# Performance work log

Hardware: AMD Instinct MI355X
Metric: run time of the kernel (lower is better)

Reference implementation:

```python
import jax, jax.numpy as jnp
import numpy as np

N = 20000        # nodes
E = 160000       # directed edges (self-loops added in reference, as PyG GATConv does)
IN = 128         # in_channels
OUT = 128        # out_channels
H = 36           # heads of conv1 (head kwarg)
C = 36           # per-head channels of conv1 (== head kwarg)
HID = H * C      # 1296, conv1 concat output
NEG_SLOPE = 0.2  # PyG GATConv default


def gat_layer(x, src, dst, W, a_src, a_dst, bias, heads, ch, concat, num_nodes):
    """One PyG-style GATConv (eval mode, self-loops already in src/dst)."""
    h = (x @ W).reshape(num_nodes, heads, ch)               # [N,H,C]
    alpha_s = jnp.sum(h * a_src, axis=-1)                   # [N,H]
    alpha_d = jnp.sum(h * a_dst, axis=-1)                   # [N,H]
    e = jax.nn.leaky_relu(alpha_s[src] + alpha_d[dst], NEG_SLOPE)  # [E,H]
    # segment softmax over incoming edges of each target node
    m = jax.ops.segment_max(e, dst, num_segments=num_nodes)        # [N,H]
    m = jnp.where(jnp.isfinite(m), m, 0.0)                  # nodes with no in-edges
    ex = jnp.exp(e - m[dst])                                # [E,H]
    denom = jax.ops.segment_sum(ex, dst, num_segments=num_nodes)   # [N,H]
    alpha = ex / (denom[dst] + 1e-16)                       # [E,H]
    # weighted scatter-aggregate of source features
    out = jax.ops.segment_sum(h[src] * alpha[:, :, None], dst, num_segments=num_nodes)  # [N,H,C]
    out = out.reshape(num_nodes, heads * ch) if concat else out.mean(axis=1)
    return out + bias


def setup_inputs() -> dict:
    key = jax.random.key(0)
    ks = jax.random.split(key, 12)
    x = jax.random.normal(ks[0], (N, IN), jnp.float32)
    edge_index = jax.random.randint(ks[1], (2, E), 0, N, dtype=jnp.int64)
    # conv1 params: heads=36, out per head=36, concat
    W1 = jax.random.normal(ks[2], (IN, H * C), jnp.float32) / np.float32(np.sqrt(IN))
    a_src1 = jax.random.normal(ks[3], (H, C), jnp.float32) * 0.1
    a_dst1 = jax.random.normal(ks[4], (H, C), jnp.float32) * 0.1
    b1 = jnp.zeros((HID,), jnp.float32)
    # conv2 params: heads=1, out=OUT, no concat
    W2 = jax.random.normal(ks[5], (HID, OUT), jnp.float32) / np.float32(np.sqrt(HID))
    a_src2 = jax.random.normal(ks[6], (1, OUT), jnp.float32) * 0.1
    a_dst2 = jax.random.normal(ks[7], (1, OUT), jnp.float32) * 0.1
    b2 = jnp.zeros((OUT,), jnp.float32)
    return {"x": x, "edge_index": edge_index,
            "W1": W1, "a_src1": a_src1, "a_dst1": a_dst1, "b1": b1,
            "W2": W2, "a_src2": a_src2, "a_dst2": a_dst2, "b2": b2}


def reference(x, edge_index, W1, a_src1, a_dst1, b1, W2, a_src2, a_dst2, b2):
    num_nodes = x.shape[0]
    loop = jnp.arange(num_nodes, dtype=edge_index.dtype)
    src = jnp.concatenate([edge_index[0], loop])   # add self-loops (PyG default)
    dst = jnp.concatenate([edge_index[1], loop])
    h = jax.nn.relu(gat_layer(x, src, dst, W1, a_src1, a_dst1, b1,
                              heads=H, ch=C, concat=True, num_nodes=num_nodes))
    out = jax.nn.relu(gat_layer(h, src, dst, W2, a_src2, a_dst2, b2,
                                heads=1, ch=OUT, concat=False, num_nodes=num_nodes))
    return out
```

## Files before the change

kernel.cpp:

```cpp
#include <hip/hip_runtime.h>

#define N_NODES 20000
#define E_EDGES 160000
#define ET (E_EDGES + N_NODES)
#define IN_CH 128
#define HID 1296
#define HEADS 36
#define CPH 36
#define OUT_CH 128
#define KP2 1344
#define NEG_SLOPE 0.2f

typedef __attribute__((ext_vector_type(8))) short bf16x8;
typedef __attribute__((ext_vector_type(8))) unsigned short ushort8;
typedef __attribute__((ext_vector_type(4))) float floatx4;

__device__ __forceinline__ float bf2f(unsigned short u) {
    union { unsigned int i; float f; } c; c.i = ((unsigned int)u) << 16; return c.f;
}
__device__ __forceinline__ unsigned short f2bf(float f) {
    union { float f; unsigned int i; } c; c.f = f;
    unsigned int r = c.i + 0x7FFF + ((c.i >> 16) & 1);
    return (unsigned short)(r >> 16);
}

#define NX (N_NODES * IN_CH / 4)
#define NW1 (HID * IN_CH)
#define NW2 (OUT_CH * KP2)
#define NPREP (NX + NW1 + NW2)
__global__ __launch_bounds__(256) void k_prepcnt(const float* __restrict__ x,
                                                 unsigned short* __restrict__ xb,
                                                 const float* __restrict__ W1,
                                                 unsigned short* __restrict__ W1T,
                                                 const float* __restrict__ W2,
                                                 unsigned short* __restrict__ W2T,
                                                 const int* __restrict__ ei,
                                                 int* __restrict__ cnt) {
    int gid = blockIdx.x * 256 + threadIdx.x;
    if (gid < NX) {
        float4 v = ((const float4*)x)[gid];
        ushort4 o; o.x = f2bf(v.x); o.y = f2bf(v.y); o.z = f2bf(v.z); o.w = f2bf(v.w);
        ((ushort4*)xb)[gid] = o;
    } else if (gid < NX + NW1) {
        int g = gid - NX;
        int n = g >> 7, k = g & 127;
        W1T[g] = f2bf(W1[(size_t)k * HID + n]);
    } else if (gid < NPREP) {
        int g = gid - NX - NW1;
        int n = g / KP2, k = g - n * KP2;
        W2T[g] = (k < HID) ? f2bf(W2[(size_t)k * OUT_CH + n]) : 0;
    } else if (gid < NPREP + ET) {
        int e = gid - NPREP;
        int d = (e < E_EDGES) ? ei[E_EDGES + e] : (e - E_EDGES);
        atomicAdd(&cnt[d], 1);
    }
}

__global__ __launch_bounds__(256) void k_gemm1(const unsigned short* __restrict__ xb,
                                               const unsigned short* __restrict__ W1T,
                                               unsigned short* __restrict__ h1b) {
    __shared__ unsigned short As[128][136];
    __shared__ unsigned short Bs[64][136];
    int tid = threadIdx.x;
    int r0 = blockIdx.x * 128;
    int n0 = blockIdx.y * 64;
#pragma unroll
    for (int i = 0; i < 8; i++) {
        int c = tid + i * 256;
        int row = c >> 4, kc = (c & 15) * 8;
        int gr = min(r0 + row, N_NODES - 1);
        *(bf16x8*)&As[row][kc] = *(const bf16x8*)(xb + (size_t)gr * IN_CH + kc);
    }
#pragma unroll
    for (int i = 0; i < 4; i++) {
        int c = tid + i * 256;
        int row = c >> 4, kc = (c & 15) * 8;
        int gn = min(n0 + row, HID - 1);
        *(bf16x8*)&Bs[row][kc] = *(const bf16x8*)(W1T + (size_t)gn * IN_CH + kc);
    }
    __syncthreads();
    int lane = tid & 63, w = tid >> 6;
    int quad = lane >> 4, l15 = lane & 15;
    int mbase = w * 32;
    floatx4 acc[2][4];
#pragma unroll
    for (int i = 0; i < 2; i++)
#pragma unroll
        for (int j = 0; j < 4; j++) acc[i][j] = (floatx4){0.f, 0.f, 0.f, 0.f};
#pragma unroll
    for (int kc = 0; kc < 128; kc += 32) {
        bf16x8 a0 = *(const bf16x8*)&As[mbase + l15][kc + quad * 8];
        bf16x8 a1 = *(const bf16x8*)&As[mbase + 16 + l15][kc + quad * 8];
#pragma unroll
        for (int j = 0; j < 4; j++) {
            bf16x8 b = *(const bf16x8*)&Bs[j * 16 + l15][kc + quad * 8];
            acc[0][j] = __builtin_amdgcn_mfma_f32_16x16x32_bf16(a0, b, acc[0][j], 0, 0, 0);
            acc[1][j] = __builtin_amdgcn_mfma_f32_16x16x32_bf16(a1, b, acc[1][j], 0, 0, 0);
        }
    }
#pragma unroll
    for (int i = 0; i < 2; i++)
#pragma unroll
        for (int j = 0; j < 4; j++) {
            int colc = n0 + j * 16 + l15;
            if (colc >= HID) continue;
#pragma unroll
            for (int r = 0; r < 4; r++) {
                int row = r0 + mbase + i * 16 + quad * 4 + r;
                if (row < N_NODES)
                    h1b[(size_t)row * HID + colc] = f2bf(acc[i][j][r]);
            }
        }
}

__global__ __launch_bounds__(256) void k_gemm2(const unsigned short* __restrict__ A,
                                               const unsigned short* __restrict__ W2T,
                                               float* __restrict__ h2a,
                                               float* __restrict__ h2b) {
    __shared__ unsigned short As[32][40];
    __shared__ unsigned short Bs[128][40];
    int tid = threadIdx.x;
    int r0 = blockIdx.x * 32;
    int kbase = blockIdx.y * 672;
    int lane = tid & 63, w = tid >> 6;
    int quad = lane >> 4, l15 = lane & 15;
    int nbase = w * 32;
    floatx4 acc[2][2];
#pragma unroll
    for (int i = 0; i < 2; i++)
#pragma unroll
        for (int j = 0; j < 2; j++) acc[i][j] = (floatx4){0.f, 0.f, 0.f, 0.f};

    for (int it = 0; it < 21; it++) {
        int k0 = kbase + it * 32;
        __syncthreads();
        if (tid < 128) {
            int row = tid >> 2, kc = (tid & 3) * 8;
            *(bf16x8*)&As[row][kc] = *(const bf16x8*)(A + (size_t)(r0 + row) * KP2 + k0 + kc);
        }
#pragma unroll
        for (int i = 0; i < 2; i++) {
            int c = tid + i * 256;
            int row = c >> 2, kc = (c & 3) * 8;
            *(bf16x8*)&Bs[row][kc] = *(const bf16x8*)(W2T + (size_t)row * KP2 + k0 + kc);
        }
        __syncthreads();
        bf16x8 a0 = *(const bf16x8*)&As[l15][quad * 8];
        bf16x8 a1 = *(const bf16x8*)&As[16 + l15][quad * 8];
        bf16x8 b0 = *(const bf16x8*)&Bs[nbase + l15][quad * 8];
        bf16x8 b1 = *(const bf16x8*)&Bs[nbase + 16 + l15][quad * 8];
        acc[0][0] = __builtin_amdgcn_mfma_f32_16x16x32_bf16(a0, b0, acc[0][0], 0, 0, 0);
        acc[1][0] = __builtin_amdgcn_mfma_f32_16x16x32_bf16(a1, b0, acc[1][0], 0, 0, 0);
        acc[0][1] = __builtin_amdgcn_mfma_f32_16x16x32_bf16(a0, b1, acc[0][1], 0, 0, 0);
        acc[1][1] = __builtin_amdgcn_mfma_f32_16x16x32_bf16(a1, b1, acc[1][1], 0, 0, 0);
    }
    float* dst = (blockIdx.y == 0) ? h2a : h2b;
#pragma unroll
    for (int i = 0; i < 2; i++)
#pragma unroll
        for (int j = 0; j < 2; j++) {
            int colc = nbase + j * 16 + l15;
#pragma unroll
            for (int r = 0; r < 4; r++) {
                int row = r0 + i * 16 + quad * 4 + r;
                dst[(size_t)row * OUT_CH + colc] = acc[i][j][r];
            }
        }
}

__global__ __launch_bounds__(256) void k_alpha1(const unsigned short* __restrict__ h1b,
                                                const float* __restrict__ a_src,
                                                const float* __restrict__ a_dst,
                                                float* __restrict__ as,
                                                float* __restrict__ ad) {
    __shared__ float s_a[HEADS * CPH], s_b[HEADS * CPH];
    int tid = threadIdx.x;
    for (int i = tid; i < HEADS * CPH; i += 256) { s_a[i] = a_src[i]; s_b[i] = a_dst[i]; }
    __syncthreads();
    int gid = blockIdx.x * 256 + tid;
    if (gid >= N_NODES * HEADS) return;
    int n = gid / HEADS, h = gid - n * HEADS;
    const unsigned short* row = h1b + (size_t)n * HID + h * CPH;
    float ss = 0.f, sd = 0.f;
#pragma unroll
    for (int c = 0; c < CPH; c += 2) {
        uint u = *(const uint*)(row + c);
        float v0 = bf2f((unsigned short)(u & 0xFFFF));
        float v1 = bf2f((unsigned short)(u >> 16));
        ss += v0 * s_a[h * CPH + c] + v1 * s_a[h * CPH + c + 1];
        sd += v0 * s_b[h * CPH + c] + v1 * s_b[h * CPH + c + 1];
    }
    as[gid] = ss;
    ad[gid] = sd;
}

__global__ __launch_bounds__(1024) void k_scan(const int* __restrict__ cnt, int* __restrict__ rowp) {
    __shared__ int sh[1024];
    const int PER = 20;
    int t = threadIdx.x;
    int base = t * PER;
    int local[PER];
    int sum = 0;
    for (int i = 0; i < PER; i++) {
        int idx = base + i;
        int v = (idx < N_NODES) ? cnt[idx] : 0;
        local[i] = sum;
        sum += v;
    }
    sh[t] = sum;
    __syncthreads();
    for (int off = 1; off < 1024; off <<= 1) {
        int v = (t >= off) ? sh[t - off] : 0;
        __syncthreads();
        sh[t] += v;
        __syncthreads();
    }
    int offset = (t == 0) ? 0 : sh[t - 1];
    for (int i = 0; i < PER; i++) {
        int idx = base + i;
        if (idx < N_NODES) rowp[idx] = offset + local[i];
    }
    if (t == 1023) rowp[N_NODES] = sh[1023];
}

__global__ void k_fill(const int* __restrict__ ei, const int* __restrict__ rowp,
                       int* __restrict__ cursor, int* __restrict__ col,
                       int* __restrict__ dstn) {
    int e = blockIdx.x * 256 + threadIdx.x;
    if (e >= ET) return;
    int s, d;
    if (e < E_EDGES) { s = ei[e]; d = ei[E_EDGES + e]; }
    else { s = e - E_EDGES; d = s; }
    int pos = rowp[d] + atomicAdd(&cursor[d], 1);
    col[pos] = s;
    dstn[pos] = d;
}

__global__ __launch_bounds__(256) void k_w1(const float* __restrict__ as1,
                                            const float* __restrict__ ad1,
                                            const int* __restrict__ col,
                                            const int* __restrict__ dstn,
                                            float* __restrict__ w,
                                            float* __restrict__ den) {
    int gid = blockIdx.x * 256 + threadIdx.x;
    if (gid >= ET * HEADS) return;
    int p = gid / HEADS, h = gid - p * HEADS;
    int s = col[p], d = dstn[p];
    float v = as1[(size_t)s * HEADS + h] + ad1[(size_t)d * HEADS + h];
    v = (v > 0.f) ? v : NEG_SLOPE * v;
    float ev = __expf(v);
    w[gid] = ev;
    atomicAdd(&den[(size_t)d * HEADS + h], ev);
}

__global__ __launch_bounds__(192) void k_agg1(const unsigned short* __restrict__ h1b,
                                              const float* __restrict__ w,
                                              const float* __restrict__ den,
                                              const int* __restrict__ rowp,
                                              const int* __restrict__ col,
                                              const float* __restrict__ b1,
                                              unsigned short* __restrict__ out1b) {
    int n = blockIdx.x;
    int tid = threadIdx.x;
    int r0 = rowp[n], r1 = rowp[n + 1];
    const bool act = tid < 162;
    int c0 = tid * 8;
    int h0 = act ? c0 / 36 : 0;
    int h7 = act ? (c0 + 7) / 36 : 0;
    int split = (h0 + 1) * 36 - c0;
    float sel[8];
#pragma unroll
    for (int j = 0; j < 8; j++) sel[j] = (j < split) ? 0.f : 1.f;
    float inv0 = 0.f, inv7 = 0.f;
    if (act) {
        inv0 = 1.f / (den[(size_t)n * HEADS + h0] + 1e-16f);
        inv7 = (h7 == h0) ? inv0 : 1.f / (den[(size_t)n * HEADS + h7] + 1e-16f);
    }
    float acc[8];
#pragma unroll
    for (int j = 0; j < 8; j++) acc[j] = 0.f;

    if (act) {
        int e = r0;
        for (; e + 4 <= r1; e += 4) {
            int s0 = col[e], s1 = col[e + 1], s2 = col[e + 2], s3 = col[e + 3];
            float wA0 = w[(size_t)(e + 0) * HEADS + h0] * inv0;
            float wB0 = w[(size_t)(e + 0) * HEADS + h7] * inv7;
            float wA1 = w[(size_t)(e + 1) * HEADS + h0] * inv0;
            float wB1 = w[(size_t)(e + 1) * HEADS + h7] * inv7;
            float wA2 = w[(size_t)(e + 2) * HEADS + h0] * inv0;
            float wB2 = w[(size_t)(e + 2) * HEADS + h7] * inv7;
            float wA3 = w[(size_t)(e + 3) * HEADS + h0] * inv0;
            float wB3 = w[(size_t)(e + 3) * HEADS + h7] * inv7;
            ushort8 v0 = *(const ushort8*)(h1b + (size_t)s0 * HID + c0);
            ushort8 v1 = *(const ushort8*)(h1b + (size_t)s1 * HID + c0);
            ushort8 v2 = *(const ushort8*)(h1b + (size_t)s2 * HID + c0);
            ushort8 v3 = *(const ushort8*)(h1b + (size_t)s3 * HID + c0);
            float dw0 = wB0 - wA0, dw1 = wB1 - wA1, dw2 = wB2 - wA2, dw3 = wB3 - wA3;
#pragma unroll
            for (int j = 0; j < 8; j++) {
                acc[j] = fmaf(fmaf(sel[j], dw0, wA0), bf2f(v0[j]), acc[j]);
                acc[j] = fmaf(fmaf(sel[j], dw1, wA1), bf2f(v1[j]), acc[j]);
                acc[j] = fmaf(fmaf(sel[j], dw2, wA2), bf2f(v2[j]), acc[j]);
                acc[j] = fmaf(fmaf(sel[j], dw3, wA3), bf2f(v3[j]), acc[j]);
            }
        }
        for (; e < r1; e++) {
            int s = col[e];
            float wA = w[(size_t)e * HEADS + h0] * inv0;
            float wB = w[(size_t)e * HEADS + h7] * inv7;
            ushort8 vv = *(const ushort8*)(h1b + (size_t)s * HID + c0);
            float dw = wB - wA;
#pragma unroll
            for (int j = 0; j < 8; j++)
                acc[j] = fmaf(fmaf(sel[j], dw, wA), bf2f(vv[j]), acc[j]);
        }
    }
    if (tid < KP2 / 8) {
        ushort8 o;
        if (act) {
#pragma unroll
            for (int j = 0; j < 8; j++) {
                float vv = acc[j] + b1[c0 + j];
                o[j] = f2bf(fmaxf(vv, 0.f));
            }
        } else {
#pragma unroll
            for (int j = 0; j < 8; j++) o[j] = 0;
        }
        *(ushort8*)(out1b + (size_t)n * KP2 + c0) = o;
    }
}

__global__ __launch_bounds__(64) void k_alpha2c(const float* __restrict__ h2a,
                                                const float* __restrict__ h2b,
                                                unsigned short* __restrict__ h2q,
                                                const float* __restrict__ a_src,
                                                const float* __restrict__ a_dst,
                                                float* __restrict__ as,
                                                float* __restrict__ ad) {
    int n = blockIdx.x;
    int t = threadIdx.x;
    size_t base = (size_t)n * OUT_CH;
    float v0 = h2a[base + t] + h2b[base + t];
    float v1 = h2a[base + t + 64] + h2b[base + t + 64];
    h2q[base + t] = f2bf(v0);
    h2q[base + t + 64] = f2bf(v1);
    float ss = v0 * a_src[t] + v1 * a_src[t + 64];
    float sd = v0 * a_dst[t] + v1 * a_dst[t + 64];
    for (int off = 32; off > 0; off >>= 1) {
        ss += __shfl_down(ss, off);
        sd += __shfl_down(sd, off);
    }
    if (t == 0) { as[n] = ss; ad[n] = sd; }
}

__global__ __launch_bounds__(64) void k_agg2(const unsigned short* __restrict__ h2q,
                                             const float* __restrict__ as,
                                             const float* __restrict__ ad,
                                             const int* __restrict__ rowp,
                                             const int* __restrict__ col,
                                             const float* __restrict__ b2,
                                             float* __restrict__ out) {
    int n = blockIdx.x;
    int t = threadIdx.x;
    int r0 = rowp[n], r1 = rowp[n + 1];
    float adn = ad[n];
    float den = 0.f;
    for (int e = r0 + t; e < r1; e += 64) {
        float v = as[col[e]] + adn;
        v = (v > 0.f) ? v : NEG_SLOPE * v;
        den += __expf(v);
    }
#pragma unroll
    for (int off = 32; off > 0; off >>= 1) den += __shfl_xor(den, off);
    float inv = 1.f / (den + 1e-16f);
    __shared__ float wsh[32];
    __shared__ int csh[32];
    float acc0 = 0.f, acc1 = 0.f;
    for (int p0 = r0; p0 < r1; p0 += 32) {
        int ne = min(32, r1 - p0);
        __syncthreads();
        if (t < ne) {
            int s = col[p0 + t];
            csh[t] = s;
            float v = as[s] + adn;
            v = (v > 0.f) ? v : NEG_SLOPE * v;
            wsh[t] = __expf(v) * inv;
        }
        __syncthreads();
        int e = 0;
        for (; e + 4 <= ne; e += 4) {
            uint u0 = *(const uint*)(h2q + (size_t)csh[e + 0] * OUT_CH + t * 2);
            uint u1 = *(const uint*)(h2q + (size_t)csh[e + 1] * OUT_CH + t * 2);
            uint u2 = *(const uint*)(h2q + (size_t)csh[e + 2] * OUT_CH + t * 2);
            uint u3 = *(const uint*)(h2q + (size_t)csh[e + 3] * OUT_CH + t * 2);
            float w0 = wsh[e], w1 = wsh[e + 1], w2 = wsh[e + 2], w3 = wsh[e + 3];
            acc0 += w0 * bf2f((unsigned short)(u0 & 0xFFFF)) + w1 * bf2f((unsigned short)(u1 & 0xFFFF))
                  + w2 * bf2f((unsigned short)(u2 & 0xFFFF)) + w3 * bf2f((unsigned short)(u3 & 0xFFFF));
            acc1 += w0 * bf2f((unsigned short)(u0 >> 16)) + w1 * bf2f((unsigned short)(u1 >> 16))
                  + w2 * bf2f((unsigned short)(u2 >> 16)) + w3 * bf2f((unsigned short)(u3 >> 16));
        }
        for (; e < ne; e++) {
            uint ua = *(const uint*)(h2q + (size_t)csh[e] * OUT_CH + t * 2);
            float wa = wsh[e];
            acc0 += wa * bf2f((unsigned short)(ua & 0xFFFF));
            acc1 += wa * bf2f((unsigned short)(ua >> 16));
        }
    }
    float o0 = acc0 + b2[t * 2];
    float o1 = acc1 + b2[t * 2 + 1];
    out[(size_t)n * OUT_CH + t * 2]     = (o0 > 0.f) ? o0 : 0.f;
    out[(size_t)n * OUT_CH + t * 2 + 1] = (o1 > 0.f) ? o1 : 0.f;
}

extern "C" void kernel_launch(void* const* d_in, const int* in_sizes, int n_in,
                              void* d_out, int out_size, void* d_ws, size_t ws_size,
                              hipStream_t stream) {
    const float* x      = (const float*)d_in[0];
    const int*   ei     = (const int*)d_in[1];
    const float* W1     = (const float*)d_in[2];
    const float* a_src1 = (const float*)d_in[3];
    const float* a_dst1 = (const float*)d_in[4];
    const float* b1     = (const float*)d_in[5];
    const float* W2     = (const float*)d_in[6];
    const float* a_src2 = (const float*)d_in[7];
    const float* a_dst2 = (const float*)d_in[8];
    const float* b2     = (const float*)d_in[9];
    float* out = (float*)d_out;

    unsigned short* h1b   = (unsigned short*)d_ws;
    unsigned short* out1b = h1b + (size_t)N_NODES * HID;
    unsigned short* xb    = out1b + (size_t)N_NODES * KP2;
    unsigned short* W1T   = xb + (size_t)N_NODES * IN_CH;
    unsigned short* W2T   = W1T + (size_t)HID * IN_CH;
    float* fbase = (float*)(W2T + NW2);
    float* as1  = fbase;
    float* ad1  = as1 + (size_t)N_NODES * HEADS;
    float* wbuf = ad1 + (size_t)N_NODES * HEADS;
    float* h2a  = wbuf;
    float* h2b  = wbuf + (size_t)N_NODES * OUT_CH;
    unsigned short* h2q = (unsigned short*)(wbuf + (size_t)2 * N_NODES * OUT_CH);
    float* as2  = wbuf + (size_t)ET * HEADS;
    float* ad2  = as2 + N_NODES;
    int* cnt    = (int*)(ad2 + N_NODES);
    int* cursor = cnt + N_NODES;
    float* den1 = (float*)(cursor + N_NODES);
    int* rowp   = (int*)(den1 + (size_t)N_NODES * HEADS);
    int* colx   = rowp + (N_NODES + 1);
    int* dstn   = colx + ET;

    hipMemsetAsync(cnt, 0, (size_t)(2 * N_NODES + N_NODES * HEADS) * sizeof(int), stream);

    k_prepcnt<<<(NPREP + ET + 255) / 256, 256, 0, stream>>>(x, xb, W1, W1T, W2, W2T, ei, cnt);
    k_scan<<<1, 1024, 0, stream>>>(cnt, rowp);
    k_fill<<<(ET + 255) / 256, 256, 0, stream>>>(ei, rowp, cursor, colx, dstn);
    k_gemm1<<<dim3(157, 21), 256, 0, stream>>>(xb, W1T, h1b);
    k_alpha1<<<(N_NODES * HEADS + 255) / 256, 256, 0, stream>>>(h1b, a_src1, a_dst1, as1, ad1);
    k_w1<<<(ET * HEADS + 255) / 256, 256, 0, stream>>>(as1, ad1, colx, dstn, wbuf, den1);
    k_agg1<<<N_NODES, 192, 0, stream>>>(h1b, wbuf, den1, rowp, colx, b1, out1b);
    k_gemm2<<<dim3(625, 2), 256, 0, stream>>>(out1b, W2T, h2a, h2b);
    k_alpha2c<<<N_NODES, 64, 0, stream>>>(h2a, h2b, h2q, a_src2, a_dst2, as2, ad2);
    k_agg2<<<N_NODES, 64, 0, stream>>>(h2q, as2, ad2, rowp, colx, b2, out);
}
```

Baseline: 316.5 us.

## Fuse attention-weight softmax into aggregation kernels with deferred normalization

Removes the separate per-edge-per-head weight kernel and its atomic denominator accumulation. Layer-1 aggregation now computes exp(leaky_relu(as+ad)) inline from node-level scores and normalizes by the accumulated sum at the end. Layer-2 aggregation likewise drops its separate denominator pass and normalizes after accumulation. This saves a large weight buffer write/read, atomics and a memset, at the cost of recomputing exponentials redundantly across threads in each block.

```diff
diff --git a/kernel.cpp b/kernel.cpp
--- a/kernel.cpp
+++ b/kernel.cpp
@@ -22,6 +22,9 @@
     union { float f; unsigned int i; } c; c.f = f;
     unsigned int r = c.i + 0x7FFF + ((c.i >> 16) & 1);
     return (unsigned short)(r >> 16);
+}
+__device__ __forceinline__ float lrelu(float v) {
+    return (v > 0.f) ? v : NEG_SLOPE * v;
 }
 
 #define NX (N_NODES * IN_CH / 4)
@@ -224,8 +227,7 @@
 }
 
 __global__ void k_fill(const int* __restrict__ ei, const int* __restrict__ rowp,
-                       int* __restrict__ cursor, int* __restrict__ col,
-                       int* __restrict__ dstn) {
+                       int* __restrict__ cursor, int* __restrict__ col) {
     int e = blockIdx.x * 256 + threadIdx.x;
     if (e >= ET) return;
     int s, d;
@@ -233,29 +235,11 @@
     else { s = e - E_EDGES; d = s; }
     int pos = rowp[d] + atomicAdd(&cursor[d], 1);
     col[pos] = s;
-    dstn[pos] = d;
-}
-
-__global__ __launch_bounds__(256) void k_w1(const float* __restrict__ as1,
-                                            const float* __restrict__ ad1,
-                                            const int* __restrict__ col,
-                                            const int* __restrict__ dstn,
-                                            float* __restrict__ w,
-                                            float* __restrict__ den) {
-    int gid = blockIdx.x * 256 + threadIdx.x;
-    if (gid >= ET * HEADS) return;
-    int p = gid / HEADS, h = gid - p * HEADS;
-    int s = col[p], d = dstn[p];
-    float v = as1[(size_t)s * HEADS + h] + ad1[(size_t)d * HEADS + h];
-    v = (v > 0.f) ? v : NEG_SLOPE * v;
-    float ev = __expf(v);
-    w[gid] = ev;
-    atomicAdd(&den[(size_t)d * HEADS + h], ev);
 }
 
 __global__ __launch_bounds__(192) void k_agg1(const unsigned short* __restrict__ h1b,
-                                              const float* __restrict__ w,
-                                              const float* __restrict__ den,
+                                              const float* __restrict__ as1,
+                                              const float* __restrict__ ad1,
                                               const int* __restrict__ rowp,
                                               const int* __restrict__ col,
                                               const float* __restrict__ b1,
@@ -271,31 +255,34 @@
     float sel[8];
 #pragma unroll
     for (int j = 0; j < 8; j++) sel[j] = (j < split) ? 0.f : 1.f;
-    float inv0 = 0.f, inv7 = 0.f;
+    float ad0 = 0.f, ad7 = 0.f;
     if (act) {
-        inv0 = 1.f / (den[(size_t)n * HEADS + h0] + 1e-16f);
-        inv7 = (h7 == h0) ? inv0 : 1.f / (den[(size_t)n * HEADS + h7] + 1e-16f);
+        ad0 = ad1[(size_t)n * HEADS + h0];
+        ad7 = (h7 == h0) ? ad0 : ad1[(size_t)n * HEADS + h7];
     }
     float acc[8];
 #pragma unroll
     for (int j = 0; j < 8; j++) acc[j] = 0.f;
+    float sA = 0.f, sB = 0.f;
 
     if (act) {
         int e = r0;
         for (; e + 4 <= r1; e += 4) {
             int s0 = col[e], s1 = col[e + 1], s2 = col[e + 2], s3 = col[e + 3];
-            float wA0 = w[(size_t)(e + 0) * HEADS + h0] * inv0;
-            float wB0 = w[(size_t)(e + 0) * HEADS + h7] * inv7;
-            float wA1 = w[(size_t)(e + 1) * HEADS + h0] * inv0;
-            float wB1 = w[(size_t)(e + 1) * HEADS + h7] * inv7;
-            float wA2 = w[(size_t)(e + 2) * HEADS + h0] * inv0;
-            float wB2 = w[(size_t)(e + 2) * HEADS + h7] * inv7;
-            float wA3 = w[(size_t)(e + 3) * HEADS + h0] * inv0;
-            float wB3 = w[(size_t)(e + 3) * HEADS + h7] * inv7;
+            float wA0 = __expf(lrelu(as1[(size_t)s0 * HEADS + h0] + ad0));
+            float wB0 = __expf(lrelu(as1[(size_t)s0 * HEADS + h7] + ad7));
+            float wA1 = __expf(lrelu(as1[(size_t)s1 * HEADS + h0] + ad0));
+            float wB1 = __expf(lrelu(as1[(size_t)s1 * HEADS + h7] + ad7));
+            float wA2 = __expf(lrelu(as1[(size_t)s2 * HEADS + h0] + ad0));
+            float wB2 = __expf(lrelu(as1[(size_t)s2 * HEADS + h7] + ad7));
+            float wA3 = __expf(lrelu(as1[(size_t)s3 * HEADS + h0] + ad0));
+            float wB3 = __expf(lrelu(as1[(size_t)s3 * HEADS + h7] + ad7));
             ushort8 v0 = *(const ushort8*)(h1b + (size_t)s0 * HID + c0);
             ushort8 v1 = *(const ushort8*)(h1b + (size_t)s1 * HID + c0);
             ushort8 v2 = *(const ushort8*)(h1b + (size_t)s2 * HID + c0);
             ushort8 v3 = *(const ushort8*)(h1b + (size_t)s3 * HID + c0);
+            sA += wA0 + wA1 + wA2 + wA3;
+            sB += wB0 + wB1 + wB2 + wB3;
             float dw0 = wB0 - wA0, dw1 = wB1 - wA1, dw2 = wB2 - wA2, dw3 = wB3 - wA3;
 #pragma unroll
             for (int j = 0; j < 8; j++) {
@@ -307,9 +294,10 @@
         }
         for (; e < r1; e++) {
             int s = col[e];
-            float wA = w[(size_t)e * HEADS + h0] * inv0;
-            float wB = w[(size_t)e * HEADS + h7] * inv7;
+            float wA = __expf(lrelu(as1[(size_t)s * HEADS + h0] + ad0));
+            float wB = __expf(lrelu(as1[(size_t)s * HEADS + h7] + ad7));
             ushort8 vv = *(const ushort8*)(h1b + (size_t)s * HID + c0);
+            sA += wA; sB += wB;
             float dw = wB - wA;
 #pragma unroll
             for (int j = 0; j < 8; j++)
@@ -319,9 +307,12 @@
     if (tid < KP2 / 8) {
         ushort8 o;
         if (act) {
+            float invA = 1.f / (sA + 1e-16f);
+            float invB = 1.f / (sB + 1e-16f);
+            float dinv = invB - invA;
 #pragma unroll
             for (int j = 0; j < 8; j++) {
-                float vv = acc[j] + b1[c0 + j];
+                float vv = acc[j] * fmaf(sel[j], dinv, invA) + b1[c0 + j];
                 o[j] = f2bf(fmaxf(vv, 0.f));
             }
         } else {
@@ -366,27 +357,17 @@
     int t = threadIdx.x;
     int r0 = rowp[n], r1 = rowp[n + 1];
     float adn = ad[n];
-    float den = 0.f;
-    for (int e = r0 + t; e < r1; e += 64) {
-        float v = as[col[e]] + adn;
-        v = (v > 0.f) ? v : NEG_SLOPE * v;
-        den += __expf(v);
-    }
-#pragma unroll
-    for (int off = 32; off > 0; off >>= 1) den += __shfl_xor(den, off);
-    float inv = 1.f / (den + 1e-16f);
     __shared__ float wsh[32];
     __shared__ int csh[32];
     float acc0 = 0.f, acc1 = 0.f;
+    float sw = 0.f;
     for (int p0 = r0; p0 < r1; p0 += 32) {
         int ne = min(32, r1 - p0);
         __syncthreads();
         if (t < ne) {
             int s = col[p0 + t];
             csh[t] = s;
-            float v = as[s] + adn;
-            v = (v > 0.f) ? v : NEG_SLOPE * v;
-            wsh[t] = __expf(v) * inv;
+            wsh[t] = __expf(lrelu(as[s] + adn));
         }
         __syncthreads();
         int e = 0;
@@ -396,6 +377,7 @@
             uint u2 = *(const uint*)(h2q + (size_t)csh[e + 2] * OUT_CH + t * 2);
             uint u3 = *(const uint*)(h2q + (size_t)csh[e + 3] * OUT_CH + t * 2);
             float w0 = wsh[e], w1 = wsh[e + 1], w2 = wsh[e + 2], w3 = wsh[e + 3];
+            sw += w0 + w1 + w2 + w3;
             acc0 += w0 * bf2f((unsigned short)(u0 & 0xFFFF)) + w1 * bf2f((unsigned short)(u1 & 0xFFFF))
                   + w2 * bf2f((unsigned short)(u2 & 0xFFFF)) + w3 * bf2f((unsigned short)(u3 & 0xFFFF));
             acc1 += w0 * bf2f((unsigned short)(u0 >> 16)) + w1 * bf2f((unsigned short)(u1 >> 16))
@@ -404,12 +386,14 @@
         for (; e < ne; e++) {
             uint ua = *(const uint*)(h2q + (size_t)csh[e] * OUT_CH + t * 2);
             float wa = wsh[e];
+            sw += wa;
             acc0 += wa * bf2f((unsigned short)(ua & 0xFFFF));
             acc1 += wa * bf2f((unsigned short)(ua >> 16));
         }
     }
-    float o0 = acc0 + b2[t * 2];
-    float o1 = acc1 + b2[t * 2 + 1];
+    float inv = 1.f / (sw + 1e-16f);
+    float o0 = acc0 * inv + b2[t * 2];
+    float o1 = acc1 * inv + b2[t * 2 + 1];
     out[(size_t)n * OUT_CH + t * 2]     = (o0 > 0.f) ? o0 : 0.f;
     out[(size_t)n * OUT_CH + t * 2 + 1] = (o1 > 0.f) ? o1 : 0.f;
 }
@@ -437,28 +421,24 @@
     float* fbase = (float*)(W2T + NW2);
     float* as1  = fbase;
     float* ad1  = as1 + (size_t)N_NODES * HEADS;
-    float* wbuf = ad1 + (size_t)N_NODES * HEADS;
-    float* h2a  = wbuf;
-    float* h2b  = wbuf + (size_t)N_NODES * OUT_CH;
-    unsigned short* h2q = (unsigned short*)(wbuf + (size_t)2 * N_NODES * OUT_CH);
-    float* as2  = wbuf + (size_t)ET * HEADS;
+    float* h2a  = ad1 + (size_t)N_NODES * HEADS;
+    float* h2b  = h2a + (size_t)N_NODES * OUT_CH;
+    unsigned short* h2q = (unsigned short*)(h2b + (size_t)N_NODES * OUT_CH);
+    float* as2  = (float*)(h2q + (size_t)N_NODES * OUT_CH);
     float* ad2  = as2 + N_NODES;
     int* cnt    = (int*)(ad2 + N_NODES);
     int* cursor = cnt + N_NODES;
-    float* den1 = (float*)(cursor + N_NODES);
-    int* rowp   = (int*)(den1 + (size_t)N_NODES * HEADS);
+    int* rowp   = cursor + N_NODES;
     int* colx   = rowp + (N_NODES + 1);
-    int* dstn   = colx + ET;
-
-    hipMemsetAsync(cnt, 0, (size_t)(2 * N_NODES + N_NODES * HEADS) * sizeof(int), stream);
+
+    hipMemsetAsync(cnt, 0, (size_t)(2 * N_NODES) * sizeof(int), stream);
 
     k_prepcnt<<<(NPREP + ET + 255) / 256, 256, 0, stream>>>(x, xb, W1, W1T, W2, W2T, ei, cnt);
     k_scan<<<1, 1024, 0, stream>>>(cnt, rowp);
-    k_fill<<<(ET + 255) / 256, 256, 0, stream>>>(ei, rowp, cursor, colx, dstn);
+    k_fill<<<(ET + 255) / 256, 256, 0, stream>>>(ei, rowp, cursor, colx);
     k_gemm1<<<dim3(157, 21), 256, 0, stream>>>(xb, W1T, h1b);
     k_alpha1<<<(N_NODES * HEADS + 255) / 256, 256, 0, stream>>>(h1b, a_src1, a_dst1, as1, ad1);
-    k_w1<<<(ET * HEADS + 255) / 256, 256, 0, stream>>>(as1, ad1, colx, dstn, wbuf, den1);
-    k_agg1<<<N_NODES, 192, 0, stream>>>(h1b, wbuf, den1, rowp, colx, b1, out1b);
+    k_agg1<<<N_NODES, 192, 0, stream>>>(h1b, as1, ad1, rowp, colx, b1, out1b);
     k_gemm2<<<dim3(625, 2), 256, 0, stream>>>(out1b, W2T, h2a, h2b);
     k_alpha2c<<<N_NODES, 64, 0, stream>>>(h2a, h2b, h2q, a_src2, a_dst2, as2, ad2);
     k_agg2<<<N_NODES, 64, 0, stream>>>(h2q, as2, ad2, rowp, colx, b2, out);
```

Measured after the change: 275.6 us. -12.9%, faster.
